# Optimization experiments

Hardware: AMD Instinct MI355X
Metric: run time of the kernel (lower is better)

Reference implementation:

```python
import jax, jax.numpy as jnp
import numpy as np

EPS = 1e-5

def conv3x3(x, w, b):
    # x: [B,C,H,W], w: [O,I,3,3]
    y = jax.lax.conv_general_dilated(x, w, window_strides=(1, 1),
                                     padding=((1, 1), (1, 1)),
                                     dimension_numbers=('NCHW', 'OIHW', 'NCHW'))
    return y + b[None, :, None, None]

def batchnorm(x, gamma, beta):
    # training-mode BN: batch stats over (N,H,W), biased variance
    mean = jnp.mean(x, axis=(0, 2, 3), keepdims=True)
    var = jnp.mean((x - mean) ** 2, axis=(0, 2, 3), keepdims=True)
    xn = (x - mean) * jax.lax.rsqrt(var + EPS)
    return xn * gamma[None, :, None, None] + beta[None, :, None, None]

def setup_inputs() -> dict:
    key = jax.random.key(0)
    ks = jax.random.split(key, 5)
    B, C, H, W = 4, 256, 64, 64
    fan = C * 9
    return {
        'x': jax.random.normal(ks[0], (B, C, H, W), jnp.float32),
        'wv': jax.random.normal(ks[1], (C, C, 3, 3), jnp.float32) / np.sqrt(fan),
        'bv': jax.random.normal(ks[2], (C,), jnp.float32) * 0.01,
        'gv': jnp.ones((C,), jnp.float32),
        'betav': jnp.zeros((C,), jnp.float32),
        'ww': jax.random.normal(ks[3], (C, C, 3, 3), jnp.float32) / np.sqrt(fan),
        'bw': jax.random.normal(ks[4], (C,), jnp.float32) * 0.01,
        'gw': jnp.ones((C,), jnp.float32),
        'betaw': jnp.zeros((C,), jnp.float32),
    }

def reference(x, wv, bv, gv, betav, ww, bw, gw, betaw):
    B, C, H, W = x.shape
    N = H * W
    # value branch: conv3x3 + BN -> [B, N, C]
    value = batchnorm(conv3x3(x, wv, bv), gv, betav).reshape(B, C, N)
    key_ = x.reshape(B, C, N)              # [B, C, N]
    query = key_.transpose(0, 2, 1)        # [B, N, C]
    sim = jnp.einsum('bnc,bcm->bnm', query, key_) * (C ** -0.5)  # [B, N, N]
    sim = jax.nn.softmax(sim, axis=-1)
    context = jnp.einsum('bnm,bcm->bcn', sim, value)             # [B, C, N]
    context = context.reshape(B, C, H, W)
    out = jax.nn.relu(batchnorm(conv3x3(context, ww, bw), gw, betaw))
    return out
```

## Files before the change

kernel.cpp:

```cpp
#include <hip/hip_runtime.h>
#include <cstdint>
#include <cstddef>

typedef __attribute__((ext_vector_type(8))) __bf16 bf16x8;
typedef __attribute__((ext_vector_type(4))) __bf16 bf16x4;
typedef __attribute__((ext_vector_type(4))) float  f32x4;

#define NPIX 4096
#define CHN  256

__device__ __forceinline__ void async_copy16(void* lds, const void* g) {
  __builtin_amdgcn_global_load_lds(
      (const __attribute__((address_space(1))) unsigned int*)g,
      (__attribute__((address_space(3))) unsigned int*)lds, 16, 0, 0);
}

__global__ __launch_bounds__(256) void k_transpose_cast(
    const float* __restrict__ X, __bf16* __restrict__ xT)
{
  __shared__ float tile[64][65];
  const int bid = blockIdx.x;
  const int b  = bid >> 8;
  const int pt = (bid >> 2) & 63;
  const int ct = bid & 3;
  const int tid = threadIdx.x;
  const int tc = tid & 63, tr = tid >> 6;
  const float* Xb = X + ((size_t)b*CHN + ct*64)*NPIX + pt*64;
#pragma unroll
  for (int i=0;i<16;++i) {
    int row = tr + i*4;
    tile[row][tc] = Xb[(size_t)row*NPIX + tc];
  }
  __syncthreads();
  __bf16* Tb = xT + ((size_t)b*NPIX + pt*64)*CHN + ct*64;
#pragma unroll
  for (int i=0;i<16;++i) {
    int prow = tr + i*4;
    Tb[(size_t)prow*CHN + tc] = (__bf16)tile[tc][prow];
  }
}

__global__ __launch_bounds__(256) void k_wcast(
    const float* __restrict__ wv, const float* __restrict__ ww,
    __bf16* __restrict__ wvt, __bf16* __restrict__ wwt)
{
  int idx = blockIdx.x*256 + threadIdx.x;
  int t = idx >> 16;
  int o = (idx >> 8) & 255;
  int i = idx & 255;
  size_t src = ((size_t)o*256 + i)*9 + t;
  wvt[idx] = (__bf16)wv[src];
  wwt[idx] = (__bf16)ww[src];
}

__global__ __launch_bounds__(256, 2) void k_conv_tap(
    const __bf16* __restrict__ W9,
    const __bf16* __restrict__ Bt,
    const __bf16* __restrict__ zb,
    __bf16* __restrict__ Y)
{
  __shared__ __bf16 Alds[2][64*64];
  __shared__ __bf16 Blds[2][128*64];
  const int bid0 = blockIdx.x;
  const int bid = (bid0 & 7)*64 + (bid0 >> 3);
  const int b  = bid >> 7;
  const int mt = (bid >> 5) & 3;
  const int nt = bid & 31;
  const int m0 = mt << 6;
  const int p0 = nt << 7;
  const int tid = threadIdx.x;
  const int w = tid >> 6, l = tid & 63;
  const int l15 = l & 15, lhi = l >> 4;
  const int wr = (w >> 1) << 5;
  const int wc = (w & 1) << 6;

  const __bf16* Btb = Bt + ((size_t)b << 20);
  const f32x4 vzero = {0.f,0.f,0.f,0.f};
  f32x4 acc[2][4];
#pragma unroll
  for (int i=0;i<2;++i)
#pragma unroll
    for (int j=0;j<4;++j) acc[i][j] = vzero;

  auto stage = [&](int buf, int it) {
    const int t = it >> 2, kc = it & 3;
    const int dy = t/3 - 1, dx = t%3 - 1;
    const int dq = dy*64 + dx;
    const int k0 = kc << 6;
#pragma unroll
    for (int i=0;i<2;++i) {
      int inst = w*2 + i;
      int s = inst*64 + l;
      int row = s >> 3, ch = s & 7;
      const __bf16* g = W9 + (size_t)t*65536 + (size_t)(m0+row)*256 + k0
                        + ((ch ^ (row & 7)) << 3);
      async_copy16((char*)(&Alds[buf][0]) + inst*1024, g);
    }
#pragma unroll
    for (int i=0;i<4;++i) {
      int inst = w*4 + i;
      int s = inst*64 + l;
      int pp = s >> 3, ch = s & 7;
      int p = p0 + pp;
      int xx = (p & 63) + dx;
      int yy = (p >> 6) + dy;
      bool ok = ((unsigned)xx < 64u) & ((unsigned)yy < 64u);
      const __bf16* g = ok ? (Btb + (size_t)(p + dq)*256 + k0 + ((ch ^ (pp & 7)) << 3))
                           : zb;
      async_copy16((char*)(&Blds[buf][0]) + inst*1024, g);
    }
  };

  stage(0, 0);
#pragma unroll 1
  for (int it=0; it<36; ++it) {
    const int cur = it & 1;
    if (it < 35) {
      stage(cur^1, it+1);
      asm volatile("s_waitcnt vmcnt(6)" ::: "memory");
    } else {
      asm volatile("s_waitcnt vmcnt(0)" ::: "memory");
    }
    __builtin_amdgcn_s_barrier();
    __builtin_amdgcn_sched_barrier(0);

    const char* Ac = (const char*)(&Alds[cur][0]);
    const char* Bc = (const char*)(&Blds[cur][0]);
#pragma unroll
    for (int kk=0; kk<2; ++kk) {
      const int swz = (((kk<<2)+lhi) ^ (l15 & 7)) << 4;
      bf16x8 af[2], bfr[4];
#pragma unroll
      for (int i=0;i<2;++i)
        af[i] = *(const bf16x8*)(Ac + (size_t)(wr + 16*i + l15)*128 + swz);
#pragma unroll
      for (int j=0;j<4;++j)
        bfr[j] = *(const bf16x8*)(Bc + (size_t)(wc + 16*j + l15)*128 + swz);
#pragma unroll
      for (int i=0;i<2;++i)
#pragma unroll
        for (int j=0;j<4;++j)
          acc[i][j] = __builtin_amdgcn_mfma_f32_16x16x32_bf16(af[i], bfr[j], acc[i][j], 0,0,0);
    }
    __builtin_amdgcn_s_barrier();
  }

  __bf16* Yb = Y + ((size_t)b << 20);
#pragma unroll
  for (int i=0;i<2;++i)
#pragma unroll
    for (int j=0;j<4;++j)
#pragma unroll
      for (int r=0;r<4;++r) {
        int row = m0 + wr + 16*i + lhi*4 + r;
        int col = p0 + wc + 16*j + l15;
        Yb[(size_t)row*NPIX + col] = (__bf16)acc[i][j][r];
      }
}

__global__ __launch_bounds__(256) void k_bn_stats(
    const __bf16* __restrict__ Y, const float* __restrict__ gamma,
    const float* __restrict__ beta, float* __restrict__ scale,
    float* __restrict__ shift)
{
  const int c = blockIdx.x;
  const int tid = threadIdx.x;
  float s = 0.f, s2 = 0.f;
#pragma unroll 1
  for (int b=0;b<4;++b) {
    const __bf16* p = Y + ((size_t)b*CHN + c)*NPIX;
#pragma unroll
    for (int i=0;i<2;++i) {
      bf16x8 v = *(const bf16x8*)(p + (tid + i*256)*8);
#pragma unroll
      for (int j=0;j<8;++j) { float f = (float)v[j]; s += f; s2 += f*f; }
    }
  }
#pragma unroll
  for (int d=1; d<64; d<<=1) { s += __shfl_xor(s, d, 64); s2 += __shfl_xor(s2, d, 64); }
  __shared__ float rs[4], rs2[4];
  if ((tid & 63) == 0) { rs[tid>>6] = s; rs2[tid>>6] = s2; }
  __syncthreads();
  if (tid == 0) {
    float S  = rs[0]+rs[1]+rs[2]+rs[3];
    float S2 = rs2[0]+rs2[1]+rs2[2]+rs2[3];
    const float inv_n = 1.f/16384.f;
    float mean = S*inv_n;
    float var  = S2*inv_n - mean*mean;
    float rstd = rsqrtf(var + 1e-5f);
    float sc = gamma[c]*rstd;
    scale[c] = sc;
    shift[c] = beta[c] - mean*sc;
  }
}

__global__ __launch_bounds__(256) void k_bn_apply_bf16(
    const __bf16* __restrict__ Y, const float* __restrict__ scale,
    const float* __restrict__ shift, __bf16* __restrict__ V)
{
  size_t idx = ((size_t)blockIdx.x*256 + threadIdx.x)*8;
  int c = (int)((idx >> 12) & 255);
  bf16x8 v = *(const bf16x8*)(Y + idx);
  float sc = scale[c], sh = shift[c];
  bf16x8 r;
#pragma unroll
  for (int j=0;j<8;++j) r[j] = (__bf16)((float)v[j]*sc + sh);
  *(bf16x8*)(V + idx) = r;
}

__global__ __launch_bounds__(256) void k_bn_relu(
    const __bf16* __restrict__ Y, const float* __restrict__ scale,
    const float* __restrict__ shift, float* __restrict__ out)
{
  size_t idx = ((size_t)blockIdx.x*256 + threadIdx.x)*8;
  int c = (int)((idx >> 12) & 255);
  bf16x8 v = *(const bf16x8*)(Y + idx);
  float sc = scale[c], sh = shift[c];
  float4 r0, r1;
  r0.x = fmaxf((float)v[0]*sc + sh, 0.f);
  r0.y = fmaxf((float)v[1]*sc + sh, 0.f);
  r0.z = fmaxf((float)v[2]*sc + sh, 0.f);
  r0.w = fmaxf((float)v[3]*sc + sh, 0.f);
  r1.x = fmaxf((float)v[4]*sc + sh, 0.f);
  r1.y = fmaxf((float)v[5]*sc + sh, 0.f);
  r1.z = fmaxf((float)v[6]*sc + sh, 0.f);
  r1.w = fmaxf((float)v[7]*sc + sh, 0.f);
  *(float4*)(out + idx)     = r0;
  *(float4*)(out + idx + 4) = r1;
}

__global__ __launch_bounds__(256, 1) void k_attn(
    const __bf16* __restrict__ xT,
    const __bf16* __restrict__ val,
    __bf16* __restrict__ O)
{
  __shared__ __align__(16) char smem[149504];

  const int bid0 = blockIdx.x;
  const int bid = (bid0 & 7)*32 + (bid0 >> 3);
  const int b  = bid >> 6;
  const int q0 = (bid & 63) << 6;
  const int tid = threadIdx.x;
  const int w = tid >> 6, l = tid & 63;
  const int l15 = l & 15, lhi = l >> 4;
  const int qh  = w & 1;
  const int kvh = w >> 1;

  const __bf16* xTb = xT  + ((size_t)b << 20);
  const __bf16* vb  = val + ((size_t)b << 20);

  bf16x8 aq[2][8];
#pragma unroll
  for (int rg=0; rg<2; ++rg) {
    const __bf16* qp = xTb + (size_t)(q0 + qh*32 + rg*16 + l15)*256 + lhi*8;
#pragma unroll
    for (int kc=0; kc<8; ++kc) {
      bf16x8 v = *(const bf16x8*)(qp + kc*32);
#pragma unroll
      for (int j=0;j<8;++j) v[j] = (__bf16)((float)v[j] * 0.0625f);
      aq[rg][kc] = v;
    }
  }

  auto stage = [&](int buf, int m0) {
    char* kb = smem + buf*32768;
    char* vv = smem + 65536 + buf*32768;
#pragma unroll
    for (int i=0;i<8;++i) {
      int inst = w*8 + i;
      int s = inst*64 + l;
      int row = s >> 5, cs = s & 31;
      const __bf16* g = xTb + (size_t)(m0 + row)*256 + ((cs ^ (row & 7)) << 3);
      async_copy16(kb + inst*1024, g);
    }
#pragma unroll
    for (int i=0;i<8;++i) {
      int inst = w*8 + i;
      int s = inst*64 + l;
      int row = s >> 3, cs = s & 7;
      const __bf16* g = vb + (size_t)row*NPIX + m0 + ((cs ^ (row & 7)) << 3);
      async_copy16(vv + inst*1024, g);
    }
  };

  const f32x4 vzero = {0.f,0.f,0.f,0.f};
  float lsum[2][4];
#pragma unroll
  for (int rg=0;rg<2;++rg)
#pragma unroll
    for (int r=0;r<4;++r) lsum[rg][r] = 0.f;
  f32x4 o[2][16];
#pragma unroll
  for (int rg=0;rg<2;++rg)
#pragma unroll
    for (int cf=0; cf<16; ++cf) o[rg][cf] = vzero;

  stage(0, 0);

#pragma unroll 1
  for (int mt=0; mt<64; ++mt) {
    const int cur = mt & 1;
    asm volatile("s_waitcnt vmcnt(0)" ::: "memory");
    __builtin_amdgcn_s_barrier();
    __builtin_amdgcn_sched_barrier(0);
    if (mt < 63) stage(cur^1, (mt+1) << 6);

    const char* Kc = smem + cur*32768;
    const char* Vc = smem + 65536 + cur*32768;
    __bf16* pl = (__bf16*)(smem + 131072 + w*4608);

    f32x4 s4[2][2];
#pragma unroll
    for (int rg=0;rg<2;++rg)
#pragma unroll
      for (int mf=0;mf<2;++mf) s4[rg][mf] = vzero;
#pragma unroll
    for (int mf=0; mf<2; ++mf) {
      const int row = kvh*32 + l15 + (mf<<4);
      const char* kbase = Kc + row*512;
#pragma unroll
      for (int kc=0; kc<8; ++kc) {
        bf16x8 bk = *(const bf16x8*)(kbase + ((((kc<<2)+lhi) ^ (row&7)) << 4));
        s4[0][mf] = __builtin_amdgcn_mfma_f32_16x16x32_bf16(aq[0][kc], bk, s4[0][mf], 0,0,0);
        s4[1][mf] = __builtin_amdgcn_mfma_f32_16x16x32_bf16(aq[1][kc], bk, s4[1][mf], 0,0,0);
      }
    }

#pragma unroll
    for (int rg=0;rg<2;++rg)
#pragma unroll
      for (int r=0;r<4;++r) {
        float ps = 0.f;
#pragma unroll
        for (int mf=0; mf<2; ++mf) {
          float p = __expf(s4[rg][mf][r]);
          __bf16 pbf = (__bf16)p;
          pl[(rg*16 + lhi*4 + r)*36 + l15 + (mf<<4)] = pbf;
          ps += (float)pbf;
        }
        lsum[rg][r] += ps;
      }
    bf16x8 pa0 = *(const bf16x8*)(pl + (size_t)l15*36 + lhi*8);
    bf16x8 pa1 = *(const bf16x8*)(pl + (size_t)(16 + l15)*36 + lhi*8);

#pragma unroll
    for (int cf=0; cf<16; ++cf) {
      const int c = l15 + (cf<<4);
      const char* vbase = Vc + c*128;
      bf16x8 bv = *(const bf16x8*)(vbase + ((((kvh<<2)+lhi) ^ (c&7)) << 4));
      o[0][cf] = __builtin_amdgcn_mfma_f32_16x16x32_bf16(pa0, bv, o[0][cf], 0,0,0);
      o[1][cf] = __builtin_amdgcn_mfma_f32_16x16x32_bf16(pa1, bv, o[1][cf], 0,0,0);
    }
  }

#pragma unroll
  for (int rg=0;rg<2;++rg)
#pragma unroll
    for (int r=0;r<4;++r)
#pragma unroll
      for (int d=1; d<16; d<<=1) lsum[rg][r] += __shfl_xor(lsum[rg][r], d, 64);

  __builtin_amdgcn_s_barrier();
  float* oscr = (float*)smem;
  float* lscr = (float*)(smem + 65536);
  if (w >= 2) {
    float* od = oscr + (size_t)(w-2)*8192;
#pragma unroll
    for (int rg=0;rg<2;++rg)
#pragma unroll
      for (int cf=0;cf<16;++cf)
#pragma unroll
        for (int r=0;r<4;++r)
          od[(rg*16 + lhi*4 + r)*256 + l15 + (cf<<4)] = o[rg][cf][r];
    if (l15 == 0) {
#pragma unroll
      for (int rg=0;rg<2;++rg)
#pragma unroll
        for (int r=0;r<4;++r)
          lscr[(w-2)*32 + rg*16 + lhi*4 + r] = lsum[rg][r];
    }
  }
  asm volatile("s_waitcnt lgkmcnt(0)" ::: "memory");
  __builtin_amdgcn_s_barrier();
  if (w < 2) {
    float* od = oscr + (size_t)w*8192;
    __bf16* Ob = O + ((size_t)b << 20);
#pragma unroll
    for (int rg=0;rg<2;++rg) {
      float inv[4];
#pragma unroll
      for (int r=0;r<4;++r)
        inv[r] = 1.f / (lsum[rg][r] + lscr[w*32 + rg*16 + lhi*4 + r]);
#pragma unroll
      for (int cf=0;cf<16;++cf)
#pragma unroll
        for (int r=0;r<4;++r) {
          float vtot = o[rg][cf][r] + od[(rg*16 + lhi*4 + r)*256 + l15 + (cf<<4)];
          int row = q0 + w*32 + rg*16 + lhi*4 + r;
          Ob[(size_t)row*256 + l15 + (cf<<4)] = (__bf16)(vtot * inv[r]);
        }
    }
  }
}

extern "C" void kernel_launch(void* const* d_in, const int* in_sizes, int n_in,
                              void* d_out, int out_size, void* d_ws, size_t ws_size,
                              hipStream_t stream)
{
  const float* x     = (const float*)d_in[0];
  const float* wv    = (const float*)d_in[1];
  const float* gv    = (const float*)d_in[3];
  const float* betav = (const float*)d_in[4];
  const float* ww    = (const float*)d_in[5];
  const float* gw    = (const float*)d_in[7];
  const float* betaw = (const float*)d_in[8];
  float* out = (float*)d_out;

  char* ws = (char*)d_ws;
  __bf16* xT     = (__bf16*)(ws);
  __bf16* val    = (__bf16*)(ws + 8388608);
  __bf16* Obuf   = (__bf16*)(ws + 16777216);
  __bf16* ybuf   = (__bf16*)(ws + 25165824);
  __bf16* wvt    = (__bf16*)(ws + 33554432);
  __bf16* wwt    = (__bf16*)(ws + 34734080);
  float* scale_v = (float*)(ws + 35913728);
  float* shift_v = (float*)(ws + 35914752);
  float* scale_w = (float*)(ws + 35915776);
  float* shift_w = (float*)(ws + 35916800);
  __bf16* zbuf   = (__bf16*)(ws + 35917824);
  if (ws_size < 35918848) return;

  hipMemsetAsync(zbuf, 0, 1024, stream);

  k_transpose_cast<<<1024, 256, 0, stream>>>(x, xT);
  k_wcast<<<2304, 256, 0, stream>>>(wv, ww, wvt, wwt);

  k_conv_tap<<<512, 256, 0, stream>>>(wvt, xT, zbuf, ybuf);
  k_bn_stats<<<256, 256, 0, stream>>>(ybuf, gv, betav, scale_v, shift_v);
  k_bn_apply_bf16<<<2048, 256, 0, stream>>>(ybuf, scale_v, shift_v, val);

  k_attn<<<256, 256, 0, stream>>>(xT, val, Obuf);

  k_conv_tap<<<512, 256, 0, stream>>>(wwt, Obuf, zbuf, ybuf);
  k_bn_stats<<<256, 256, 0, stream>>>(ybuf, gw, betaw, scale_w, shift_w);
  k_bn_relu<<<2048, 256, 0, stream>>>(ybuf, scale_w, shift_w, out);
}
```

Before: 238.9 us.

## Split attention work across eight waves per block with shared P exchange

The attention kernel now runs 512 threads per block instead of 256. Each wave computes scores for 16 key rows instead of 32 and accumulates half of the output channels. Probabilities are exchanged through shared memory between wave pairs, with an extra barrier per key tile. The goal is more waves per CU to hide MFMA and LDS latency, and fewer accumulator registers per wave. The cost is an added in-loop barrier, duplicated P writes, and a wider final reduction of row sums.

```diff
diff --git a/kernel.cpp b/kernel.cpp
--- a/kernel.cpp
+++ b/kernel.cpp
@@ -229,12 +229,12 @@
   *(float4*)(out + idx + 4) = r1;
 }
 
-__global__ __launch_bounds__(256, 1) void k_attn(
+__global__ __launch_bounds__(512, 2) void k_attn(
     const __bf16* __restrict__ xT,
     const __bf16* __restrict__ val,
     __bf16* __restrict__ O)
 {
-  __shared__ __align__(16) char smem[149504];
+  __shared__ __align__(16) char smem[141312];
 
   const int bid0 = blockIdx.x;
   const int bid = (bid0 & 7)*32 + (bid0 >> 3);
@@ -244,7 +244,9 @@
   const int w = tid >> 6, l = tid & 63;
   const int l15 = l & 15, lhi = l >> 4;
   const int qh  = w & 1;
-  const int kvh = w >> 1;
+  const int kvq = w >> 1;
+  const int p   = kvq >> 1;
+  const int cfh = kvq & 1;
 
   const __bf16* xTb = xT  + ((size_t)b << 20);
   const __bf16* vb  = val + ((size_t)b << 20);
@@ -266,16 +268,16 @@
     char* kb = smem + buf*32768;
     char* vv = smem + 65536 + buf*32768;
 #pragma unroll
-    for (int i=0;i<8;++i) {
-      int inst = w*8 + i;
+    for (int i=0;i<4;++i) {
+      int inst = w*4 + i;
       int s = inst*64 + l;
       int row = s >> 5, cs = s & 31;
       const __bf16* g = xTb + (size_t)(m0 + row)*256 + ((cs ^ (row & 7)) << 3);
       async_copy16(kb + inst*1024, g);
     }
 #pragma unroll
-    for (int i=0;i<8;++i) {
-      int inst = w*8 + i;
+    for (int i=0;i<4;++i) {
+      int inst = w*4 + i;
       int s = inst*64 + l;
       int row = s >> 3, cs = s & 7;
       const __bf16* g = vb + (size_t)row*NPIX + m0 + ((cs ^ (row & 7)) << 3);
@@ -289,11 +291,11 @@
   for (int rg=0;rg<2;++rg)
 #pragma unroll
     for (int r=0;r<4;++r) lsum[rg][r] = 0.f;
-  f32x4 o[2][16];
+  f32x4 o[2][8];
 #pragma unroll
   for (int rg=0;rg<2;++rg)
 #pragma unroll
-    for (int cf=0; cf<16; ++cf) o[rg][cf] = vzero;
+    for (int cf=0; cf<8; ++cf) o[rg][cf] = vzero;
 
   stage(0, 0);
 
@@ -307,47 +309,43 @@
 
     const char* Kc = smem + cur*32768;
     const char* Vc = smem + 65536 + cur*32768;
-    __bf16* pl = (__bf16*)(smem + 131072 + w*4608);
-
-    f32x4 s4[2][2];
+    __bf16* pReg = (__bf16*)(smem + 131072 + (qh*2 + p)*2560);
+
+    f32x4 s4[2];
+    s4[0] = vzero; s4[1] = vzero;
+    {
+      const int krow = kvq*16 + l15;
+      const char* kbase = Kc + krow*512;
+#pragma unroll
+      for (int kc=0; kc<8; ++kc) {
+        bf16x8 bk = *(const bf16x8*)(kbase + ((((kc<<2)+lhi) ^ (krow&7)) << 4));
+        s4[0] = __builtin_amdgcn_mfma_f32_16x16x32_bf16(aq[0][kc], bk, s4[0], 0,0,0);
+        s4[1] = __builtin_amdgcn_mfma_f32_16x16x32_bf16(aq[1][kc], bk, s4[1], 0,0,0);
+      }
+    }
+
 #pragma unroll
     for (int rg=0;rg<2;++rg)
 #pragma unroll
-      for (int mf=0;mf<2;++mf) s4[rg][mf] = vzero;
-#pragma unroll
-    for (int mf=0; mf<2; ++mf) {
-      const int row = kvh*32 + l15 + (mf<<4);
-      const char* kbase = Kc + row*512;
-#pragma unroll
-      for (int kc=0; kc<8; ++kc) {
-        bf16x8 bk = *(const bf16x8*)(kbase + ((((kc<<2)+lhi) ^ (row&7)) << 4));
-        s4[0][mf] = __builtin_amdgcn_mfma_f32_16x16x32_bf16(aq[0][kc], bk, s4[0][mf], 0,0,0);
-        s4[1][mf] = __builtin_amdgcn_mfma_f32_16x16x32_bf16(aq[1][kc], bk, s4[1][mf], 0,0,0);
+      for (int r=0;r<4;++r) {
+        float pv = __expf(s4[rg][r]);
+        __bf16 pbf = (__bf16)pv;
+        pReg[(rg*16 + lhi*4 + r)*40 + cfh*16 + l15] = pbf;
+        lsum[rg][r] += (float)pbf;
       }
-    }
-
-#pragma unroll
-    for (int rg=0;rg<2;++rg)
-#pragma unroll
-      for (int r=0;r<4;++r) {
-        float ps = 0.f;
-#pragma unroll
-        for (int mf=0; mf<2; ++mf) {
-          float p = __expf(s4[rg][mf][r]);
-          __bf16 pbf = (__bf16)p;
-          pl[(rg*16 + lhi*4 + r)*36 + l15 + (mf<<4)] = pbf;
-          ps += (float)pbf;
-        }
-        lsum[rg][r] += ps;
-      }
-    bf16x8 pa0 = *(const bf16x8*)(pl + (size_t)l15*36 + lhi*8);
-    bf16x8 pa1 = *(const bf16x8*)(pl + (size_t)(16 + l15)*36 + lhi*8);
-
-#pragma unroll
-    for (int cf=0; cf<16; ++cf) {
-      const int c = l15 + (cf<<4);
+
+    asm volatile("s_waitcnt lgkmcnt(0)" ::: "memory");
+    __builtin_amdgcn_s_barrier();
+    __builtin_amdgcn_sched_barrier(0);
+
+    bf16x8 pa0 = *(const bf16x8*)(pReg + (size_t)l15*40 + lhi*8);
+    bf16x8 pa1 = *(const bf16x8*)(pReg + (size_t)(16 + l15)*40 + lhi*8);
+
+#pragma unroll
+    for (int cf=0; cf<8; ++cf) {
+      const int c = cfh*128 + (cf<<4) + l15;
       const char* vbase = Vc + c*128;
-      bf16x8 bv = *(const bf16x8*)(vbase + ((((kvh<<2)+lhi) ^ (c&7)) << 4));
+      bf16x8 bv = *(const bf16x8*)(vbase + ((((p<<2)+lhi) ^ (c&7)) << 4));
       o[0][cf] = __builtin_amdgcn_mfma_f32_16x16x32_bf16(pa0, bv, o[0][cf], 0,0,0);
       o[1][cf] = __builtin_amdgcn_mfma_f32_16x16x32_bf16(pa1, bv, o[1][cf], 0,0,0);
     }
@@ -363,41 +361,46 @@
   __builtin_amdgcn_s_barrier();
   float* oscr = (float*)smem;
   float* lscr = (float*)(smem + 65536);
-  if (w >= 2) {
-    float* od = oscr + (size_t)(w-2)*8192;
+  if (l15 == 0) {
 #pragma unroll
     for (int rg=0;rg<2;++rg)
 #pragma unroll
-      for (int cf=0;cf<16;++cf)
+      for (int r=0;r<4;++r)
+        lscr[w*32 + rg*16 + lhi*4 + r] = lsum[rg][r];
+  }
+  if (p == 1) {
+    float* od = oscr + (size_t)(qh*2 + cfh)*4096;
+#pragma unroll
+    for (int rg=0;rg<2;++rg)
+#pragma unroll
+      for (int cf=0;cf<8;++cf)
 #pragma unroll
         for (int r=0;r<4;++r)
-          od[(rg*16 + lhi*4 + r)*256 + l15 + (cf<<4)] = o[rg][cf][r];
-    if (l15 == 0) {
-#pragma unroll
-      for (int rg=0;rg<2;++rg)
-#pragma unroll
-        for (int r=0;r<4;++r)
-          lscr[(w-2)*32 + rg*16 + lhi*4 + r] = lsum[rg][r];
-    }
+          od[(rg*16 + lhi*4 + r)*128 + (cf<<4) + l15] = o[rg][cf][r];
   }
   asm volatile("s_waitcnt lgkmcnt(0)" ::: "memory");
   __builtin_amdgcn_s_barrier();
-  if (w < 2) {
-    float* od = oscr + (size_t)w*8192;
+  if (p == 0) {
+    const float* od = oscr + (size_t)(qh*2 + cfh)*4096;
     __bf16* Ob = O + ((size_t)b << 20);
 #pragma unroll
     for (int rg=0;rg<2;++rg) {
       float inv[4];
 #pragma unroll
-      for (int r=0;r<4;++r)
-        inv[r] = 1.f / (lsum[rg][r] + lscr[w*32 + rg*16 + lhi*4 + r]);
-#pragma unroll
-      for (int cf=0;cf<16;++cf)
+      for (int r=0;r<4;++r) {
+        float tot = 0.f;
+#pragma unroll
+        for (int k=0;k<4;++k)
+          tot += lscr[(qh + 2*k)*32 + rg*16 + lhi*4 + r];
+        inv[r] = 1.f / tot;
+      }
+#pragma unroll
+      for (int cf=0;cf<8;++cf)
 #pragma unroll
         for (int r=0;r<4;++r) {
-          float vtot = o[rg][cf][r] + od[(rg*16 + lhi*4 + r)*256 + l15 + (cf<<4)];
-          int row = q0 + w*32 + rg*16 + lhi*4 + r;
-          Ob[(size_t)row*256 + l15 + (cf<<4)] = (__bf16)(vtot * inv[r]);
+          float vtot = o[rg][cf][r] + od[(rg*16 + lhi*4 + r)*128 + (cf<<4) + l15];
+          int row = q0 + qh*32 + rg*16 + lhi*4 + r;
+          Ob[(size_t)row*256 + cfh*128 + (cf<<4) + l15] = (__bf16)(vtot * inv[r]);
         }
     }
   }
@@ -439,7 +442,7 @@
   k_bn_stats<<<256, 256, 0, stream>>>(ybuf, gv, betav, scale_v, shift_v);
   k_bn_apply_bf16<<<2048, 256, 0, stream>>>(ybuf, scale_v, shift_v, val);
 
-  k_attn<<<256, 256, 0, stream>>>(xT, val, Obuf);
+  k_attn<<<256, 512, 0, stream>>>(xT, val, Obuf);
 
   k_conv_tap<<<512, 256, 0, stream>>>(wwt, Obuf, zbuf, ybuf);
   k_bn_stats<<<256, 256, 0, stream>>>(ybuf, gw, betaw, scale_w, shift_w);
```

Measured after the change: 199.5 us. 1.2x faster.
